# Kernel optimization log

Measured on AMD Instinct MI355X. Metric: run time of the kernel, lower is better.

The kernel has to match this reference:

```python
import jax, jax.numpy as jnp
import numpy as np

R, C = 8192, 8192  # dense shape of the layer's parameter tensor
NE, NN = 4_000_000, 4_000_000


def setup_inputs() -> dict:
    key = jax.random.key(0)
    k1, k2, k3, k4 = jax.random.split(key, 4)
    vals_e = jax.random.normal(k1, (NE,), dtype=jnp.float32)
    vals_n = jax.random.normal(k2, (NN,), dtype=jnp.float32)
    idx_e = jax.random.randint(k3, (2, NE), 0, R, dtype=jnp.int64)
    idx_n = jax.random.randint(k4, (2, NN), 0, R, dtype=jnp.int64)
    return {"vals_e": vals_e, "vals_n": vals_n, "idx_e": idx_e, "idx_n": idx_n}


def reference(vals_e, vals_n, idx_e, idx_n):
    # Sparse COO union with max-abs dedup, expressed as a vectorized
    # scatter-reduce into the dense parameter space (equivalent math:
    # at every index, keep the value with the largest absolute value;
    # untouched positions are 0, matching a sparse representation).
    flat_e = idx_e[0] * C + idx_e[1]  # [NE]
    flat_n = idx_n[0] * C + idx_n[1]  # [NN]
    flat = jnp.concatenate([flat_e, flat_n])            # [NE+NN]
    vals = jnp.concatenate([vals_e, vals_n])            # [NE+NN]

    # pass 1: max |v| per position
    amax = jnp.zeros((R * C,), dtype=vals.dtype).at[flat].max(jnp.abs(vals))
    # pass 2: recover the signed winner (strict-abs winner; ties measure-zero for randn)
    is_winner = jnp.abs(vals) == amax[flat]
    neg_inf = jnp.array(-jnp.inf, dtype=vals.dtype)
    cand = jnp.where(is_winner, vals, neg_inf)
    out = jnp.full((R * C,), neg_inf, dtype=vals.dtype).at[flat].max(cand)
    out = jnp.where(jnp.isneginf(out), jnp.zeros((), dtype=vals.dtype), out)
    return out.reshape(R, C)
```

## Files before the change

### kernel.cpp

```cpp
#include <hip/hip_runtime.h>

#define CDIM     8192
#define NBKT     512
#define BSH      4
#define SLOTS    32
#define SSTR     33
#define PB       8192
#define BINTHR   1024
#define PPT      20
#define MTHR     1024
#define CAP      (PPT * MTHR)
#define CSTRIDE  16
#define TWORDS   32768
#define SUBS     4

typedef int          vi4 __attribute__((ext_vector_type(4)));
typedef float        vf4 __attribute__((ext_vector_type(4)));
typedef unsigned int vu4 __attribute__((ext_vector_type(4)));

#define NTL(p)    __builtin_nontemporal_load(p)
#define NTS(p, v) __builtin_nontemporal_store((v), (p))

__global__ __launch_bounds__(1024) void k_zcnt(unsigned int* __restrict__ g) {
    g[(size_t)blockIdx.x * 1024 + threadIdx.x] = 0u;
}


__global__ __launch_bounds__(BINTHR) void k_bin_v(
    const float* __restrict__ ve, const int* __restrict__ ie, int ne,
    const float* __restrict__ vn, const int* __restrict__ in_, int nn,
    uint2* __restrict__ pairs, unsigned int* __restrict__ gcount)
{
    __shared__ uint2 stage[NBKT * SSTR];
    __shared__ unsigned int hist[NBKT];
    __shared__ unsigned int sbase[NBKT];
    const int tid = threadIdx.x;
    const int total = ne + nn;
    const int start = blockIdx.x * PB;
    const int end = min(total, start + PB);

    for (int b = tid; b < NBKT; b += BINTHR) hist[b] = 0;

    const int iA = start + tid * 4;
    const int iB = iA + BINTHR * 4;
    const bool hasA = iA < end;
    const bool hasB = iB < end;
    vi4 rvA = {0,0,0,0}, cvA = {0,0,0,0}, rvB = {0,0,0,0}, cvB = {0,0,0,0};
    vf4 xvA = {0,0,0,0}, xvB = {0,0,0,0};
    if (hasA) {
        if (iA < ne) {
            rvA = NTL((const vi4*)(ie + iA));
            cvA = NTL((const vi4*)(ie + ne + iA));
            xvA = NTL((const vf4*)(ve + iA));
        } else {
            int j = iA - ne;
            rvA = NTL((const vi4*)(in_ + j));
            cvA = NTL((const vi4*)(in_ + nn + j));
            xvA = NTL((const vf4*)(vn + j));
        }
    }
    if (hasB) {
        if (iB < ne) {
            rvB = NTL((const vi4*)(ie + iB));
            cvB = NTL((const vi4*)(ie + ne + iB));
            xvB = NTL((const vf4*)(ve + iB));
        } else {
            int j = iB - ne;
            rvB = NTL((const vi4*)(in_ + j));
            cvB = NTL((const vi4*)(in_ + nn + j));
            xvB = NTL((const vf4*)(vn + j));
        }
    }
    __syncthreads();

    #pragma unroll
    for (int it = 0; it < 2; ++it) {
        const bool has = it == 0 ? hasA : hasB;
        if (!has) continue;
        const int i0 = it == 0 ? iA : iB;
        const vi4 rv = it == 0 ? rvA : rvB;
        const vi4 cv = it == 0 ? cvA : cvB;
        const vf4 xv = it == 0 ? xvA : xvB;
        const int lim = end - i0;
        #pragma unroll
        for (int q = 0; q < 4; ++q) {
            if (q < lim) {
                int r = rv[q];
                int c = cv[q];
                unsigned int u = __float_as_uint(xv[q]);
                unsigned int key = ((u & 0x7FFFFFFFu) << 1) | (u >> 31);
                if (key) {
                    unsigned int b = (unsigned int)r >> BSH;
                    unsigned int off = (((unsigned int)r & 15u) << 13) | (unsigned int)c;
                    unsigned int rk = atomicAdd(&hist[b], 1u);
                    if (__builtin_expect(rk < SLOTS, 1)) {
                        stage[b * SSTR + rk] = make_uint2(off, key);
                    } else {
                        unsigned int d = atomicAdd(&gcount[(size_t)b * CSTRIDE], 8u);
                        if (d + 8u <= CAP) {
                            unsigned int* dst = (unsigned int*)(pairs + (size_t)b * CAP + d);
                            vu4 w0 = {off, key, 0u, 0u};
                            vu4 z4 = {0u, 0u, 0u, 0u};
                            NTS((vu4*)(dst),      w0);
                            NTS((vu4*)(dst + 4),  z4);
                            NTS((vu4*)(dst + 8),  z4);
                            NTS((vu4*)(dst + 12), z4);
                        }
                    }
                }
            }
        }
    }
    __syncthreads();

    if (tid < NBKT) {
        unsigned int staged = min(hist[tid], (unsigned int)SLOTS);
        unsigned int rr = (staged + 7u) & ~7u;
        sbase[tid] = rr ? atomicAdd(&gcount[(size_t)tid * CSTRIDE], rr) : 0u;
        hist[tid] = staged;
    }
    __syncthreads();

    const int s = tid & 3;
    for (int b = tid >> 2; b < NBKT; b += (BINTHR >> 2)) {
        unsigned int staged = hist[b];
        unsigned int rr = (staged + 7u) & ~7u;
        unsigned int gb = sbase[b];
        for (unsigned int k = (unsigned int)(s * 2); k < rr; k += 8u) {
            uint2 v0 = (k     < staged) ? stage[b * SSTR + k]     : make_uint2(0u, 0u);
            uint2 v1 = (k + 1 < staged) ? stage[b * SSTR + k + 1] : make_uint2(0u, 0u);
            unsigned int d = gb + k;
            if (d + 2u <= CAP) {
                vu4 w = {v0.x, v0.y, v1.x, v1.y};
                NTS((vu4*)(pairs + (size_t)b * CAP + d), w);
            }
        }
    }
}

__global__ __launch_bounds__(MTHR) void k_merge(
    const uint2* __restrict__ pairs, const unsigned int* __restrict__ gcount,
    unsigned int* __restrict__ out)
{
    __shared__ unsigned int lk[TWORDS];
    const int b = blockIdx.x;
    const int tid = threadIdx.x;

    unsigned int cnt = gcount[(size_t)b * CSTRIDE];
    if (cnt > CAP) cnt = CAP;
    const vu4* p4 = (const vu4*)(pairs + (size_t)b * CAP);

    vu4 myp[PPT / 2];
    #pragma unroll
    for (int k = 0; k < PPT / 2; ++k) {
        unsigned int i2 = (unsigned int)(k * MTHR + tid);
        vu4 zz = {0u, 0u, 0u, 0u};
        myp[k] = (2u * i2 < cnt) ? NTL(p4 + i2) : zz;
    }

    vu4 z = {0u, 0u, 0u, 0u};
    for (int sub = 0; sub < SUBS; ++sub) {
        for (int i = tid; i < TWORDS / 4; i += MTHR) ((vu4*)lk)[i] = z;
        __syncthreads();
        #pragma unroll
        for (int k = 0; k < PPT / 2; ++k) {
            vu4 pr = myp[k];
            if (pr[1] && (pr[0] >> 15) == (unsigned int)sub)
                atomicMax(&lk[pr[0] & 32767u], pr[1]);
            if (pr[3] && (pr[2] >> 15) == (unsigned int)sub)
                atomicMax(&lk[pr[2] & 32767u], pr[3]);
        }
        __syncthreads();
        size_t ob = (size_t)b * 131072u + (size_t)sub * TWORDS;
        for (int i = tid; i < TWORDS / 4; i += MTHR) {
            vu4 k = ((vu4*)lk)[i];
            k[0] = (k[0] >> 1) | ((k[0] & 1u) << 31);
            k[1] = (k[1] >> 1) | ((k[1] & 1u) << 31);
            k[2] = (k[2] >> 1) | ((k[2] & 1u) << 31);
            k[3] = (k[3] >> 1) | ((k[3] & 1u) << 31);
            NTS((vu4*)(out + ob) + i, k);
        }
        __syncthreads();
    }
}


__global__ void k_zero(uint4* __restrict__ out, int n4) {
    int stride = gridDim.x * blockDim.x;
    uint4 z = {0u, 0u, 0u, 0u};
    for (int i = blockIdx.x * blockDim.x + threadIdx.x; i < n4; i += stride)
        out[i] = z;
}

__global__ void k_scatter(const float* __restrict__ vals_e,
                          const int* __restrict__ idx_e, int ne,
                          const float* __restrict__ vals_n,
                          const int* __restrict__ idx_n, int nn,
                          unsigned int* __restrict__ out) {
    int total = ne + nn;
    int stride = gridDim.x * blockDim.x;
    for (int i = blockIdx.x * blockDim.x + threadIdx.x; i < total; i += stride) {
        const float* v; const int* idx; int j, n;
        if (i < ne) { v = vals_e; idx = idx_e; j = i;      n = ne; }
        else        { v = vals_n; idx = idx_n; j = i - ne; n = nn; }
        float x = v[j];
        unsigned int u = __float_as_uint(x);
        unsigned int key = ((u & 0x7FFFFFFFu) << 1) | (u >> 31);
        if (key) {
            int r = idx[j];
            int c = idx[n + j];
            atomicMax(&out[(size_t)r * CDIM + (size_t)c], key);
        }
    }
}

__global__ void k_decode(uint4* __restrict__ out, int n4) {
    int stride = gridDim.x * blockDim.x;
    for (int i = blockIdx.x * blockDim.x + threadIdx.x; i < n4; i += stride) {
        uint4 k = out[i];
        k.x = (k.x >> 1) | ((k.x & 1u) << 31);
        k.y = (k.y >> 1) | ((k.y & 1u) << 31);
        k.z = (k.z >> 1) | ((k.z & 1u) << 31);
        k.w = (k.w >> 1) | ((k.w & 1u) << 31);
        out[i] = k;
    }
}

extern "C" void kernel_launch(void* const* d_in, const int* in_sizes, int n_in,
                              void* d_out, int out_size, void* d_ws, size_t ws_size,
                              hipStream_t stream) {
    const float* vals_e = (const float*)d_in[0];
    const float* vals_n = (const float*)d_in[1];
    const int*   idx_e  = (const int*)d_in[2];
    const int*   idx_n  = (const int*)d_in[3];
    int ne = in_sizes[0];
    int nn = in_sizes[1];
    int total = ne + nn;

    const size_t gcount_bytes = (size_t)NBKT * CSTRIDE * sizeof(unsigned int);
    const size_t pairs_bytes  = (size_t)NBKT * CAP * sizeof(uint2);
    const size_t ws_need = gcount_bytes + pairs_bytes;

    if (ws_size >= ws_need && ((ne | nn) & 3) == 0) {
        unsigned int* gcount = (unsigned int*)d_ws;
        uint2* pairs = (uint2*)((char*)d_ws + gcount_bytes);

        k_zcnt<<<dim3(NBKT * CSTRIDE / 1024), dim3(1024), 0, stream>>>(gcount);

        int nblk = (total + PB - 1) / PB;
        k_bin_v<<<dim3(nblk), dim3(BINTHR), 0, stream>>>(
            vals_e, idx_e, ne, vals_n, idx_n, nn, pairs, gcount);
        k_merge<<<dim3(NBKT), dim3(MTHR), 0, stream>>>(
            pairs, gcount, (unsigned int*)d_out);
    } else {
        unsigned int* out = (unsigned int*)d_out;
        int n4 = out_size / 4;
        dim3 block(256);
        dim3 grid(2048);
        k_zero<<<grid, block, 0, stream>>>((uint4*)d_out, n4);
        k_scatter<<<grid, block, 0, stream>>>(vals_e, idx_e, ne, vals_n, idx_n, nn, out);
        k_decode<<<grid, block, 0, stream>>>((uint4*)d_out, n4);
    }
}
```

Measured before the change: 123.2 us.

## Use fixed per-block bucket slabs with sharded overflow instead of global atomics

Each binning block now writes its staged pairs for every bucket into a fixed-position slab indexed by block id. This removes the global atomicAdd reservations per bucket and the padded per-element spill writes. Elements past the smaller slot count go to a 64-way sharded overflow list tagged with their bucket. Every merge block scans the whole overflow list on each sub-pass, so the trade is an always-written padded slab plus redundant overflow scans in exchange for far less global atomic contention.

```diff
diff --git a/kernel.cpp b/kernel.cpp
--- a/kernel.cpp
+++ b/kernel.cpp
@@ -3,16 +3,17 @@
 #define CDIM     8192
 #define NBKT     512
 #define BSH      4
-#define SLOTS    32
-#define SSTR     33
+#define SLOTS    24
+#define SSTR     25
 #define PB       8192
 #define BINTHR   1024
-#define PPT      20
 #define MTHR     1024
-#define CAP      (PPT * MTHR)
-#define CSTRIDE  16
 #define TWORDS   32768
 #define SUBS     4
+#define OVFSH    64
+#define OVFSEG   4096
+#define OVFSTR   16
+#define MYP4     12
 
 typedef int          vi4 __attribute__((ext_vector_type(4)));
 typedef float        vf4 __attribute__((ext_vector_type(4)));
@@ -21,19 +22,19 @@
 #define NTL(p)    __builtin_nontemporal_load(p)
 #define NTS(p, v) __builtin_nontemporal_store((v), (p))
 
-__global__ __launch_bounds__(1024) void k_zcnt(unsigned int* __restrict__ g) {
-    g[(size_t)blockIdx.x * 1024 + threadIdx.x] = 0u;
+__global__ __launch_bounds__(1024) void k_zinit(unsigned int* __restrict__ g) {
+    g[threadIdx.x] = 0u;
 }
 
 
 __global__ __launch_bounds__(BINTHR) void k_bin_v(
     const float* __restrict__ ve, const int* __restrict__ ie, int ne,
     const float* __restrict__ vn, const int* __restrict__ in_, int nn,
-    uint2* __restrict__ pairs, unsigned int* __restrict__ gcount)
+    uint2* __restrict__ pairs, unsigned int* __restrict__ ovfcnt,
+    uint2* __restrict__ ovf, int nblk)
 {
     __shared__ uint2 stage[NBKT * SSTR];
     __shared__ unsigned int hist[NBKT];
-    __shared__ unsigned int sbase[NBKT];
     const int tid = threadIdx.x;
     const int total = ne + nn;
     const int start = blockIdx.x * PB;
@@ -96,16 +97,11 @@
                     if (__builtin_expect(rk < SLOTS, 1)) {
                         stage[b * SSTR + rk] = make_uint2(off, key);
                     } else {
-                        unsigned int d = atomicAdd(&gcount[(size_t)b * CSTRIDE], 8u);
-                        if (d + 8u <= CAP) {
-                            unsigned int* dst = (unsigned int*)(pairs + (size_t)b * CAP + d);
-                            vu4 w0 = {off, key, 0u, 0u};
-                            vu4 z4 = {0u, 0u, 0u, 0u};
-                            NTS((vu4*)(dst),      w0);
-                            NTS((vu4*)(dst + 4),  z4);
-                            NTS((vu4*)(dst + 8),  z4);
-                            NTS((vu4*)(dst + 12), z4);
-                        }
+                        unsigned int sh = (unsigned int)blockIdx.x & (OVFSH - 1u);
+                        unsigned int d = atomicAdd(&ovfcnt[sh * OVFSTR], 1u);
+                        if (d < OVFSEG)
+                            ovf[(size_t)sh * OVFSEG + d] =
+                                make_uint2((b << 17) | off, key);
                     }
                 }
             }
@@ -113,62 +109,64 @@
     }
     __syncthreads();
 
-    if (tid < NBKT) {
-        unsigned int staged = min(hist[tid], (unsigned int)SLOTS);
-        unsigned int rr = (staged + 7u) & ~7u;
-        sbase[tid] = rr ? atomicAdd(&gcount[(size_t)tid * CSTRIDE], rr) : 0u;
-        hist[tid] = staged;
-    }
-    __syncthreads();
-
-    const int s = tid & 3;
-    for (int b = tid >> 2; b < NBKT; b += (BINTHR >> 2)) {
-        unsigned int staged = hist[b];
-        unsigned int rr = (staged + 7u) & ~7u;
-        unsigned int gb = sbase[b];
-        for (unsigned int k = (unsigned int)(s * 2); k < rr; k += 8u) {
-            uint2 v0 = (k     < staged) ? stage[b * SSTR + k]     : make_uint2(0u, 0u);
-            uint2 v1 = (k + 1 < staged) ? stage[b * SSTR + k + 1] : make_uint2(0u, 0u);
-            unsigned int d = gb + k;
-            if (d + 2u <= CAP) {
-                vu4 w = {v0.x, v0.y, v1.x, v1.y};
-                NTS((vu4*)(pairs + (size_t)b * CAP + d), w);
-            }
-        }
+    const size_t slab = (size_t)nblk * SLOTS;
+    for (int c = tid; c < NBKT * SLOTS / 2; c += BINTHR) {
+        int l0 = 2 * c;
+        int b = l0 / SLOTS;
+        int s = l0 % SLOTS;
+        unsigned int staged = min(hist[b], (unsigned int)SLOTS);
+        uint2 v0 = ((unsigned int)s     < staged) ? stage[b * SSTR + s]     : make_uint2(0u, 0u);
+        uint2 v1 = ((unsigned int)s + 1 < staged) ? stage[b * SSTR + s + 1] : make_uint2(0u, 0u);
+        vu4 w = {v0.x, v0.y, v1.x, v1.y};
+        NTS((vu4*)(pairs + (size_t)b * slab + (size_t)blockIdx.x * SLOTS + s), w);
     }
 }
 
 __global__ __launch_bounds__(MTHR) void k_merge(
-    const uint2* __restrict__ pairs, const unsigned int* __restrict__ gcount,
-    unsigned int* __restrict__ out)
+    const uint2* __restrict__ pairs, const unsigned int* __restrict__ ovfcnt,
+    const uint2* __restrict__ ovf, unsigned int* __restrict__ out, int nblk)
 {
     __shared__ unsigned int lk[TWORDS];
+    __shared__ unsigned int ovfc[OVFSH];
     const int b = blockIdx.x;
     const int tid = threadIdx.x;
 
-    unsigned int cnt = gcount[(size_t)b * CSTRIDE];
-    if (cnt > CAP) cnt = CAP;
-    const vu4* p4 = (const vu4*)(pairs + (size_t)b * CAP);
-
-    vu4 myp[PPT / 2];
+    const size_t slab = (size_t)nblk * SLOTS;
+    const int n4 = (int)(slab >> 1);
+    const vu4* p4 = (const vu4*)(pairs + (size_t)b * slab);
+
+    if (tid < OVFSH)
+        ovfc[tid] = min(ovfcnt[tid * OVFSTR], (unsigned int)OVFSEG);
+
+    vu4 myp[MYP4];
     #pragma unroll
-    for (int k = 0; k < PPT / 2; ++k) {
-        unsigned int i2 = (unsigned int)(k * MTHR + tid);
+    for (int k = 0; k < MYP4; ++k) {
+        int i2 = k * MTHR + tid;
         vu4 zz = {0u, 0u, 0u, 0u};
-        myp[k] = (2u * i2 < cnt) ? NTL(p4 + i2) : zz;
-    }
+        myp[k] = (i2 < n4) ? NTL(p4 + i2) : zz;
+    }
+    __syncthreads();
 
     vu4 z = {0u, 0u, 0u, 0u};
     for (int sub = 0; sub < SUBS; ++sub) {
         for (int i = tid; i < TWORDS / 4; i += MTHR) ((vu4*)lk)[i] = z;
         __syncthreads();
         #pragma unroll
-        for (int k = 0; k < PPT / 2; ++k) {
+        for (int k = 0; k < MYP4; ++k) {
             vu4 pr = myp[k];
             if (pr[1] && (pr[0] >> 15) == (unsigned int)sub)
                 atomicMax(&lk[pr[0] & 32767u], pr[1]);
             if (pr[3] && (pr[2] >> 15) == (unsigned int)sub)
                 atomicMax(&lk[pr[2] & 32767u], pr[3]);
+        }
+        for (int s = 0; s < OVFSH; ++s) {
+            unsigned int cs = ovfc[s];
+            for (unsigned int i = (unsigned int)tid; i < cs; i += MTHR) {
+                uint2 e = ovf[(size_t)s * OVFSEG + i];
+                unsigned int off = e.x & 0x1FFFFu;
+                if ((e.x >> 17) == (unsigned int)b && (off >> 15) == (unsigned int)sub)
+                    atomicMax(&lk[off & 32767u], e.y);
+            }
         }
         __syncthreads();
         size_t ob = (size_t)b * 131072u + (size_t)sub * TWORDS;
@@ -236,22 +234,24 @@
     int ne = in_sizes[0];
     int nn = in_sizes[1];
     int total = ne + nn;
-
-    const size_t gcount_bytes = (size_t)NBKT * CSTRIDE * sizeof(unsigned int);
-    const size_t pairs_bytes  = (size_t)NBKT * CAP * sizeof(uint2);
-    const size_t ws_need = gcount_bytes + pairs_bytes;
-
-    if (ws_size >= ws_need && ((ne | nn) & 3) == 0) {
-        unsigned int* gcount = (unsigned int*)d_ws;
-        uint2* pairs = (uint2*)((char*)d_ws + gcount_bytes);
-
-        k_zcnt<<<dim3(NBKT * CSTRIDE / 1024), dim3(1024), 0, stream>>>(gcount);
-
-        int nblk = (total + PB - 1) / PB;
+    int nblk = (total + PB - 1) / PB;
+
+    const size_t ovfcnt_bytes = (size_t)OVFSH * OVFSTR * sizeof(unsigned int);
+    const size_t ovf_bytes    = (size_t)OVFSH * OVFSEG * sizeof(uint2);
+    const size_t pairs_bytes  = (size_t)NBKT * nblk * SLOTS * sizeof(uint2);
+    const size_t ws_need = ovfcnt_bytes + ovf_bytes + pairs_bytes;
+
+    if (ws_size >= ws_need && ((ne | nn) & 3) == 0 && nblk <= 1024) {
+        unsigned int* ovfcnt = (unsigned int*)d_ws;
+        uint2* ovf   = (uint2*)((char*)d_ws + ovfcnt_bytes);
+        uint2* pairs = (uint2*)((char*)d_ws + ovfcnt_bytes + ovf_bytes);
+
+        k_zinit<<<dim3(1), dim3(1024), 0, stream>>>(ovfcnt);
+
         k_bin_v<<<dim3(nblk), dim3(BINTHR), 0, stream>>>(
-            vals_e, idx_e, ne, vals_n, idx_n, nn, pairs, gcount);
+            vals_e, idx_e, ne, vals_n, idx_n, nn, pairs, ovfcnt, ovf, nblk);
         k_merge<<<dim3(NBKT), dim3(MTHR), 0, stream>>>(
-            pairs, gcount, (unsigned int*)d_out);
+            pairs, ovfcnt, ovf, (unsigned int*)d_out, nblk);
     } else {
         unsigned int* out = (unsigned int*)d_out;
         int n4 = out_size / 4;
```

Result: slower. 228.9 us (+85.8%).
